# Kernel optimization log

Hardware: AMD Instinct MI355X
Metric: run time of the kernel (lower is better)

Reference implementation:

```python
import jax, jax.numpy as jnp
import numpy as np

B, L, D, H = 32, 512, 512, 8          # batch(=num_nodes), seq len, model_size, num_heads
HD = D // H                            # head size
E_DIM, N_EDGES, N_PATHS = 128, 4096, 1024  # edge_dim (hardcoded 128), edge table, #(src,dst) pairs
MAXD = H                               # max_path_distance == num_heads


def setup_inputs() -> dict:
    rng = jax.random.key(0)
    ks = jax.random.split(rng, 16)
    n = lambda k, s: jax.random.normal(k, s, jnp.float32)
    idx = jnp.arange(N_PATHS)
    inp = {
        'query': n(ks[0], (B, L, D)),
        'key':   n(ks[1], (B, L, D)),
        'value': n(ks[2], (B, L, D)),
        'mask':  jnp.ones((B, 1, 1, L), jnp.float32),
        'edge_attr': n(ks[3], (N_EDGES, E_DIM)),
        'path_src': (idx // B).astype(jnp.int32),   # all (src,dst) node pairs
        'path_dst': (idx % B).astype(jnp.int32),
        'path_edges': jax.random.randint(ks[4], (N_PATHS, MAXD), 0, N_EDGES),
        'path_lens': jax.random.randint(ks[5], (N_PATHS,), 1, MAXD + 1),
        # learned params
        'WQ': n(ks[6], (D, D)) * 0.02, 'bQ': jnp.zeros((D,), jnp.float32),
        'WK': n(ks[7], (D, D)) * 0.02, 'bK': jnp.zeros((D,), jnp.float32),
        'WV': n(ks[8], (D, D)) * 0.02, 'bV': jnp.zeros((D,), jnp.float32),
        'WO': n(ks[9], (D, D)) * 0.02, 'bO': jnp.zeros((D,), jnp.float32),
        'edge_vector': n(ks[10], (MAXD, E_DIM)) * 0.05,  # EdgeEncoding weight
        'b_vec': n(ks[11], (MAXD,)) * 0.05,              # SpatialEncoding weight
        'b_scale': jnp.float32(0.001),
        'c_scale': jnp.float32(0.001),
    }
    return inp


def reference(query, key, value, mask, edge_attr, path_src, path_dst, path_edges,
              path_lens, WQ, bQ, WK, bK, WV, bV, WO, bO, edge_vector, b_vec,
              b_scale, c_scale):
    def split_heads(x):  # [B,L,D] -> [B,H,L,HD]
        return x.reshape(B, L, H, HD).transpose(0, 2, 1, 3)

    q = split_heads(jnp.einsum('bld,de->ble', query, WQ) + bQ)
    k = split_heads(jnp.einsum('bld,de->ble', key, WK) + bK)
    v = split_heads(jnp.einsum('bld,de->ble', value, WV) + bV)

    score = jnp.einsum('bhqd,bhkd->bhqk', q, k) / jnp.sqrt(jnp.float32(HD))

    pl = jnp.minimum(path_lens, MAXD).astype(jnp.int32)  # clipped path lengths

    # SpatialEncoding: spatial[src,dst] = b_vec[min(len,maxd)-1]
    spatial = jnp.zeros((B, B), jnp.float32).at[path_src, path_dst].set(b_vec[pl - 1])
    b_mean = spatial.mean(axis=1)  # [B]

    # EdgeEncoding: cij[src,dst] = mean_k <edge_vector[k], edge_attr[path[k]]>
    pe = edge_attr[path_edges]                       # [P,MAXD,E]  batched gather
    dots = jnp.einsum('ke,pke->pk', edge_vector, pe)  # [P,MAXD]
    kmask = (jnp.arange(MAXD)[None, :] < pl[:, None]).astype(jnp.float32)
    cvals = jnp.where(pl > 0, (dots * kmask).sum(1) / jnp.maximum(pl, 1), 0.0)
    cij = jnp.zeros((B, B), jnp.float32).at[path_src, path_dst].set(cvals)
    c_mean = cij.mean(axis=1)  # [B]

    bias = (b_scale * b_mean + c_scale * c_mean)[:, None, None, None]
    score = score + bias + (1.0 - mask) * (-1e9)

    alpha = jax.nn.softmax(score, axis=-1)
    ctx = jnp.einsum('bhqk,bhkd->bhqd', alpha, v)
    ctx = ctx.transpose(0, 2, 1, 3).reshape(B, L, D)
    return jnp.einsum('bld,de->ble', ctx, WO) + bO
```

## Files before the change

### kernel.cpp

```cpp
#include <hip/hip_runtime.h>
#include <hip/hip_bf16.h>

#define B_  32
#define L_  512
#define D_  512
#define H_  8
#define HD_ 64

typedef __attribute__((ext_vector_type(8))) short bf16x8;
typedef __attribute__((ext_vector_type(4))) short bf16x4;
typedef __attribute__((ext_vector_type(4))) float f32x4;

__device__ __forceinline__ short f2bf(float f) {
  union { float f; unsigned u; } x; x.f = f;
  unsigned r = x.u + 0x7FFFu + ((x.u >> 16) & 1u);
  return (short)(r >> 16);
}

__device__ __forceinline__ void gll16(const void* g, void* l) {
  __builtin_amdgcn_global_load_lds(
      (const __attribute__((address_space(1))) unsigned int*)g,
      (__attribute__((address_space(3))) unsigned int*)l, 16, 0, 0);
}

__device__ __forceinline__ bf16x8 cvt8(f32x4 a, f32x4 b) {
  union { __hip_bfloat162 h[4]; bf16x8 v; } u;
  u.h[0] = __float22bfloat162_rn(float2{a[0], a[1]});
  u.h[1] = __float22bfloat162_rn(float2{a[2], a[3]});
  u.h[2] = __float22bfloat162_rn(float2{b[0], b[1]});
  u.h[3] = __float22bfloat162_rn(float2{b[2], b[3]});
  return u.v;
}

#define DS_FENCE() do { asm volatile("s_waitcnt lgkmcnt(0)" ::: "memory"); \
                        __builtin_amdgcn_sched_barrier(0); } while (0)

__global__ __launch_bounds__(256) void wt_kernel(
    const float* __restrict__ WQ, const float* __restrict__ WK,
    const float* __restrict__ WV, const float* __restrict__ WO,
    short* __restrict__ wt) {
  __shared__ float tile[32][33];
  int wz = blockIdx.z;
  const float* W = (wz == 0) ? WQ : (wz == 1) ? WK : (wz == 2) ? WV : WO;
  int k0 = blockIdx.y * 32, n0 = blockIdx.x * 32;
  int tr = threadIdx.x >> 5, tc = threadIdx.x & 31;
#pragma unroll
  for (int i = 0; i < 4; ++i)
    tile[tr + i * 8][tc] = W[(size_t)(k0 + tr + i * 8) * D_ + n0 + tc];
  __syncthreads();
#pragma unroll
  for (int i = 0; i < 4; ++i)
    wt[((size_t)wz * D_ + n0 + tr + i * 8) * D_ + k0 + tc] =
        f2bf(tile[tc][tr + i * 8]);
}

__global__ __launch_bounds__(256) void gemm_qkv(
    const float* __restrict__ Xq, const float* __restrict__ Xk,
    const float* __restrict__ Xv, const short* __restrict__ wt,
    const float* __restrict__ bQ, const float* __restrict__ bK,
    const float* __restrict__ bV,
    short* __restrict__ q_ws, short* __restrict__ k_ws,
    short* __restrict__ vt_ws) {
  __shared__ __align__(16) char lds[49152];
  char* Al = lds;
  char* Bl = lds + 32768;

  int mode = blockIdx.z;
  const float* A = (mode == 0) ? Xq : (mode == 1) ? Xk : Xv;
  const short* WT = wt + (size_t)mode * D_ * D_;
  const float* bias = (mode == 0) ? bQ : (mode == 1) ? bK : bV;

  int wgid = blockIdx.x + 4 * blockIdx.y;
  int rr_ = wgid >> 3;
  int m0 = ((wgid & 7) * 16 + (rr_ >> 2)) * 128;
  int n0 = (rr_ & 3) * 128;

  int tid = threadIdx.x, lane = tid & 63, w = tid >> 6;
  int wr = w >> 1, wc = w & 1, g = lane >> 4, lr = lane & 15;

  f32x4 acc[4][4] = {};

  for (int k0 = 0; k0 < D_; k0 += 64) {
    __syncthreads();
#pragma unroll
    for (int j = 0; j < 8; ++j) {
      int e = w * 8 + j;
      int row = e * 4 + (lane >> 4);
      int chunk = (lane & 15) ^ (row & 15);
      gll16(A + (size_t)(m0 + row) * D_ + k0 + chunk * 4, Al + e * 1024);
    }
#pragma unroll
    for (int j = 0; j < 4; ++j) {
      int e = w * 4 + j;
      int row = e * 8 + (lane >> 3);
      int chunk = (lane & 7) ^ (lane >> 3);
      gll16(WT + (size_t)(n0 + row) * D_ + k0 + chunk * 8, Bl + e * 1024);
    }
    __syncthreads();
#pragma unroll
    for (int kk = 0; kk < 2; ++kk) {
      bf16x8 af[4], bf_[4];
#pragma unroll
      for (int i = 0; i < 4; ++i) {
        int row = wr * 64 + i * 16 + lr;
        int o0 = ((kk * 8 + g * 2) ^ lr) << 4;
        int o1 = ((kk * 8 + g * 2 + 1) ^ lr) << 4;
        f32x4 lo = *(const f32x4*)(Al + row * 256 + o0);
        f32x4 hi = *(const f32x4*)(Al + row * 256 + o1);
        af[i] = cvt8(lo, hi);
      }
#pragma unroll
      for (int i = 0; i < 4; ++i) {
        int row = wc * 64 + i * 16 + lr;
        bf_[i] = *(const bf16x8*)(Bl + row * 128 +
                                  (((kk * 4 + g) ^ (lr & 7)) << 4));
      }
#pragma unroll
      for (int mi = 0; mi < 4; ++mi)
#pragma unroll
        for (int nj = 0; nj < 4; ++nj)
          acc[mi][nj] = __builtin_amdgcn_mfma_f32_16x16x32_bf16(
              af[mi], bf_[nj], acc[mi][nj], 0, 0, 0);
    }
  }

#pragma unroll
  for (int mi = 0; mi < 4; ++mi) {
#pragma unroll
    for (int nj = 0; nj < 4; ++nj) {
      int n = n0 + wc * 64 + nj * 16 + lr;
      float bb = bias[n];
      int h = n >> 6, hd = n & 63;
#pragma unroll
      for (int rr = 0; rr < 4; ++rr) {
        int m = m0 + wr * 64 + mi * 16 + g * 4 + rr;
        int b = m >> 9, l = m & 511;
        short v = f2bf(acc[mi][nj][rr] + bb);
        if (mode == 0)
          q_ws[(((size_t)b * H_ + h) * L_ + l) * HD_ + hd] = v;
        else if (mode == 1)
          k_ws[(((size_t)b * H_ + h) * L_ + l) * HD_ + hd] = v;
        else
          vt_ws[(((size_t)b * H_ + h) * HD_ + hd) * L_ + l] = v;
      }
    }
  }
}

__global__ __launch_bounds__(256, 4) void attn_kernel(
    const short* __restrict__ q_ws, const short* __restrict__ k_ws,
    const short* __restrict__ vt_ws, const float* __restrict__ mask,
    short* __restrict__ ctx_ws) {
  __shared__ __align__(16) char lds[40960];
  int wg = blockIdx.x;
  int bh   = (wg & 7) * 32 + (wg >> 6);
  int qblk = (wg >> 3) & 7;
  int b = bh >> 3, h = bh & 7;
  int tid = threadIdx.x, lane = tid & 63, w = tid >> 6;
  int g = lane >> 4, lr = lane & 15;
  char* Pl = lds + 32768 + w * 2048;
  int qbase = qblk * 64 + w * 16;

  const short* Qh  = q_ws  + (size_t)bh * (L_ * HD_);
  const short* Kh  = k_ws  + (size_t)bh * (L_ * HD_);
  const short* VTh = vt_ws + (size_t)bh * (HD_ * L_);
  const float* mrow = mask + (size_t)b * L_;

  bf16x8 aq0 = *(const bf16x8*)(Qh + (size_t)(qbase + lr) * HD_ + g * 8);
  bf16x8 aq1 = *(const bf16x8*)(Qh + (size_t)(qbase + lr) * HD_ + 32 + g * 8);

  int rowin = lane >> 3;
  int sch8 = ((lane & 7) ^ rowin) * 8;

#pragma unroll
  for (int j = 0; j < 2; ++j) {
    int e = w * 2 + j, row = e * 8 + rowin;
    gll16(Kh + (size_t)row * HD_ + sch8, lds + e * 1024);
    gll16(VTh + (size_t)row * L_ + sch8, lds + 16384 + e * 1024);
  }
  __syncthreads();

  f32x4 c[4] = {};
  float m[4] = {-1e30f, -1e30f, -1e30f, -1e30f};
  float sum[4] = {0.f, 0.f, 0.f, 0.f};

  for (int ch = 0; ch < 8; ++ch) {
    const char* Kb = lds + (ch & 1) * 8192;
    const char* Vb = lds + 16384 + (ch & 1) * 8192;
    if (ch < 7) {
      char* Kn = lds + ((ch + 1) & 1) * 8192;
      char* Vn = lds + 16384 + ((ch + 1) & 1) * 8192;
#pragma unroll
      for (int j = 0; j < 2; ++j) {
        int e = w * 2 + j, row = e * 8 + rowin;
        gll16(Kh + ((size_t)(ch + 1) * 64 + row) * HD_ + sch8, Kn + e * 1024);
        gll16(VTh + (size_t)row * L_ + (ch + 1) * 64 + sch8, Vn + e * 1024);
      }
    }
    float mb[4];
#pragma unroll
    for (int kt = 0; kt < 4; ++kt)
      mb[kt] = (1.0f - mrow[ch * 64 + kt * 16 + lr]) * -1e9f;

    f32x4 s[4];
#pragma unroll
    for (int kt = 0; kt < 4; ++kt) {
      int row = kt * 16 + lr;
      bf16x8 bk0 = *(const bf16x8*)(Kb + row * 128 + ((g ^ (lr & 7)) << 4));
      bf16x8 bk1 = *(const bf16x8*)(Kb + row * 128 + (((4 + g) ^ (lr & 7)) << 4));
      f32x4 a = {0.f, 0.f, 0.f, 0.f};
      a = __builtin_amdgcn_mfma_f32_16x16x32_bf16(aq0, bk0, a, 0, 0, 0);
      a = __builtin_amdgcn_mfma_f32_16x16x32_bf16(aq1, bk1, a, 0, 0, 0);
#pragma unroll
      for (int rr = 0; rr < 4; ++rr) a[rr] = a[rr] * 0.125f + mb[kt];
      s[kt] = a;
    }

    float pmax[4], scl[4];
#pragma unroll
    for (int rr = 0; rr < 4; ++rr)
      pmax[rr] = fmaxf(fmaxf(s[0][rr], s[1][rr]), fmaxf(s[2][rr], s[3][rr]));
#pragma unroll
    for (int off = 1; off < 16; off <<= 1)
#pragma unroll
      for (int rr = 0; rr < 4; ++rr)
        pmax[rr] = fmaxf(pmax[rr], __shfl_xor(pmax[rr], off, 64));
#pragma unroll
    for (int rr = 0; rr < 4; ++rr) {
      float mn = fmaxf(m[rr], pmax[rr]);
      scl[rr] = __expf(m[rr] - mn);
      m[rr] = mn;
      sum[rr] *= scl[rr];
    }
#pragma unroll
    for (int nt = 0; nt < 4; ++nt)
#pragma unroll
      for (int rr = 0; rr < 4; ++rr) c[nt][rr] *= scl[rr];

#pragma unroll
    for (int kt = 0; kt < 4; ++kt) {
      int col2 = (kt * 16 + lr) * 2;
#pragma unroll
      for (int rr = 0; rr < 4; ++rr) {
        float p = __expf(s[kt][rr] - m[rr]);
        sum[rr] += p;
        int row = g * 4 + rr;
        *(short*)(Pl + row * 128 + (col2 ^ ((row & 7) << 4))) = f2bf(p);
      }
    }
    DS_FENCE();

#pragma unroll
    for (int kk = 0; kk < 2; ++kk) {
      bf16x8 ap = *(const bf16x8*)(Pl + lr * 128 +
                                   (((kk * 4 + g) ^ (lr & 7)) << 4));
#pragma unroll
      for (int nt = 0; nt < 4; ++nt) {
        int row = nt * 16 + lr;
        bf16x8 bv = *(const bf16x8*)(Vb + row * 128 +
                                     (((kk * 4 + g) ^ (lr & 7)) << 4));
        c[nt] = __builtin_amdgcn_mfma_f32_16x16x32_bf16(ap, bv, c[nt], 0, 0, 0);
      }
    }
    DS_FENCE();
    if (ch < 7) __syncthreads();
  }

  float inv[4];
#pragma unroll
  for (int off = 1; off < 16; off <<= 1)
#pragma unroll
    for (int rr = 0; rr < 4; ++rr) sum[rr] += __shfl_xor(sum[rr], off, 64);
#pragma unroll
  for (int rr = 0; rr < 4; ++rr) inv[rr] = 1.0f / sum[rr];

#pragma unroll
  for (int nt = 0; nt < 4; ++nt) {
    int hd = nt * 16 + lr;
#pragma unroll
    for (int rr = 0; rr < 4; ++rr) {
      int qrow = qbase + g * 4 + rr;
      ctx_ws[(((size_t)b * L_ + qrow) * H_ + h) * HD_ + hd] =
          f2bf(c[nt][rr] * inv[rr]);
    }
  }
}

__global__ __launch_bounds__(256) void gemm_out(
    const short* __restrict__ ctx, const short* __restrict__ wt3,
    const float* __restrict__ bO, float* __restrict__ out) {
  __shared__ __align__(16) char lds[32768];
  char* Al = lds;
  char* Bl = lds + 16384;
  int wgid = blockIdx.x + 4 * blockIdx.y;
  int rr_ = wgid >> 3;
  int m0 = ((wgid & 7) * 16 + (rr_ >> 2)) * 128;
  int n0 = (rr_ & 3) * 128;
  int tid = threadIdx.x, lane = tid & 63, w = tid >> 6;
  int wr = w >> 1, wc = w & 1, g = lane >> 4, lr = lane & 15;
  f32x4 acc[4][4] = {};

  for (int k0 = 0; k0 < D_; k0 += 64) {
    __syncthreads();
#pragma unroll
    for (int j = 0; j < 4; ++j) {
      int e = w * 4 + j;
      int row = e * 8 + (lane >> 3);
      int chunk = (lane & 7) ^ (lane >> 3);
      gll16(ctx + (size_t)(m0 + row) * D_ + k0 + chunk * 8, Al + e * 1024);
    }
#pragma unroll
    for (int j = 0; j < 4; ++j) {
      int e = w * 4 + j;
      int row = e * 8 + (lane >> 3);
      int chunk = (lane & 7) ^ (lane >> 3);
      gll16(wt3 + (size_t)(n0 + row) * D_ + k0 + chunk * 8, Bl + e * 1024);
    }
    __syncthreads();
#pragma unroll
    for (int kk = 0; kk < 2; ++kk) {
      bf16x8 af[4], bf_[4];
#pragma unroll
      for (int i = 0; i < 4; ++i) {
        int row = wr * 64 + i * 16 + lr;
        af[i] = *(const bf16x8*)(Al + row * 128 +
                                 (((kk * 4 + g) ^ (lr & 7)) << 4));
      }
#pragma unroll
      for (int i = 0; i < 4; ++i) {
        int row = wc * 64 + i * 16 + lr;
        bf_[i] = *(const bf16x8*)(Bl + row * 128 +
                                  (((kk * 4 + g) ^ (lr & 7)) << 4));
      }
#pragma unroll
      for (int mi = 0; mi < 4; ++mi)
#pragma unroll
        for (int nj = 0; nj < 4; ++nj)
          acc[mi][nj] = __builtin_amdgcn_mfma_f32_16x16x32_bf16(
              af[mi], bf_[nj], acc[mi][nj], 0, 0, 0);
    }
  }
#pragma unroll
  for (int mi = 0; mi < 4; ++mi) {
#pragma unroll
    for (int nj = 0; nj < 4; ++nj) {
      int n = n0 + wc * 64 + nj * 16 + lr;
      float bb = bO[n];
#pragma unroll
      for (int rr = 0; rr < 4; ++rr) {
        int m = m0 + wr * 64 + mi * 16 + g * 4 + rr;
        out[(size_t)m * D_ + n] = acc[mi][nj][rr] + bb;
      }
    }
  }
}

extern "C" void kernel_launch(void* const* d_in, const int* in_sizes, int n_in,
                              void* d_out, int out_size, void* d_ws,
                              size_t ws_size, hipStream_t stream) {
  const float* query = (const float*)d_in[0];
  const float* key   = (const float*)d_in[1];
  const float* value = (const float*)d_in[2];
  const float* mask  = (const float*)d_in[3];
  const float* WQ = (const float*)d_in[9];
  const float* bQ = (const float*)d_in[10];
  const float* WK = (const float*)d_in[11];
  const float* bK = (const float*)d_in[12];
  const float* WV = (const float*)d_in[13];
  const float* bV = (const float*)d_in[14];
  const float* WO = (const float*)d_in[15];
  const float* bO = (const float*)d_in[16];

  short* ws  = (short*)d_ws;
  short* wt  = ws;
  short* q   = ws + 1048576;
  short* k   = q + 8388608;
  short* vt  = k + 8388608;
  short* ctx = vt + 8388608;
  float* out = (float*)d_out;

  wt_kernel<<<dim3(16, 16, 4), 256, 0, stream>>>(WQ, WK, WV, WO, wt);
  gemm_qkv<<<dim3(4, 128, 3), 256, 0, stream>>>(query, key, value, wt,
                                                bQ, bK, bV, q, k, vt);
  attn_kernel<<<2048, 256, 0, stream>>>(q, k, vt, mask, ctx);
  gemm_out<<<dim3(4, 128), 256, 0, stream>>>(ctx, wt + 3 * 262144, bO, out);
}
```

Measured before the change: 135.5 us.

## Load A operand directly to registers and double-buffer B tiles in LDS

Both the QKV projection and the output projection GEMMs stop staging the activation (A) tile through LDS. Each wave now loads its A fragments straight from global memory into registers, prefetching the next K-step while the current one runs on MFMA. The weight (B) tile is double-buffered in LDS, so only one barrier per K-step is needed and the next tile's load overlaps compute. This cuts LDS traffic and footprint and adds an occupancy hint of 3 blocks, at the cost of more registers held by prefetched fragments and uncoalesced-per-wave global reads of A.

```diff
diff --git a/kernel.cpp b/kernel.cpp
--- a/kernel.cpp
+++ b/kernel.cpp
@@ -54,16 +54,14 @@
         f2bf(tile[tc][tr + i * 8]);
 }
 
-__global__ __launch_bounds__(256) void gemm_qkv(
+__global__ __launch_bounds__(256, 3) void gemm_qkv(
     const float* __restrict__ Xq, const float* __restrict__ Xk,
     const float* __restrict__ Xv, const short* __restrict__ wt,
     const float* __restrict__ bQ, const float* __restrict__ bK,
     const float* __restrict__ bV,
     short* __restrict__ q_ws, short* __restrict__ k_ws,
     short* __restrict__ vt_ws) {
-  __shared__ __align__(16) char lds[49152];
-  char* Al = lds;
-  char* Bl = lds + 32768;
+  __shared__ __align__(16) char Bl[2][16384];
 
   int mode = blockIdx.z;
   const float* A = (mode == 0) ? Xq : (mode == 1) ? Xk : Xv;
@@ -77,50 +75,83 @@
 
   int tid = threadIdx.x, lane = tid & 63, w = tid >> 6;
   int wr = w >> 1, wc = w & 1, g = lane >> 4, lr = lane & 15;
+  int rowin = lane >> 3, sch8 = ((lane & 7) ^ rowin) * 8;
+
+  const float* Ab = A + (size_t)(m0 + wr * 64 + lr) * D_ + g * 8;
 
   f32x4 acc[4][4] = {};
-
-  for (int k0 = 0; k0 < D_; k0 += 64) {
+  bf16x8 acur[4][2];
+
+#pragma unroll
+  for (int j = 0; j < 4; ++j) {
+    int e = w * 4 + j, row = e * 8 + rowin;
+    gll16(WT + (size_t)(n0 + row) * D_ + sch8, &Bl[0][e * 1024]);
+  }
+#pragma unroll
+  for (int i = 0; i < 4; ++i)
+#pragma unroll
+    for (int kk = 0; kk < 2; ++kk) {
+      const float* p = Ab + (size_t)i * (16 * D_) + kk * 32;
+      acur[i][kk] = cvt8(*(const f32x4*)p, *(const f32x4*)(p + 4));
+    }
+
+#pragma unroll
+  for (int it = 0; it < 8; ++it) {
     __syncthreads();
-#pragma unroll
-    for (int j = 0; j < 8; ++j) {
-      int e = w * 8 + j;
-      int row = e * 4 + (lane >> 4);
-      int chunk = (lane & 15) ^ (row & 15);
-      gll16(A + (size_t)(m0 + row) * D_ + k0 + chunk * 4, Al + e * 1024);
-    }
-#pragma unroll
-    for (int j = 0; j < 4; ++j) {
-      int e = w * 4 + j;
-      int row = e * 8 + (lane >> 3);
-      int chunk = (lane & 7) ^ (lane >> 3);
-      gll16(WT + (size_t)(n0 + row) * D_ + k0 + chunk * 8, Bl + e * 1024);
-    }
-    __syncthreads();
-#pragma unroll
-    for (int kk = 0; kk < 2; ++kk) {
-      bf16x8 af[4], bf_[4];
+    if (it < 7) {
+#pragma unroll
+      for (int j = 0; j < 4; ++j) {
+        int e = w * 4 + j, row = e * 8 + rowin;
+        gll16(WT + (size_t)(n0 + row) * D_ + (it + 1) * 64 + sch8,
+              &Bl[(it + 1) & 1][e * 1024]);
+      }
+    }
+    f32x4 nx0[4], nx1[4], ny0[4], ny1[4];
+    if (it < 7) {
 #pragma unroll
       for (int i = 0; i < 4; ++i) {
-        int row = wr * 64 + i * 16 + lr;
-        int o0 = ((kk * 8 + g * 2) ^ lr) << 4;
-        int o1 = ((kk * 8 + g * 2 + 1) ^ lr) << 4;
-        f32x4 lo = *(const f32x4*)(Al + row * 256 + o0);
-        f32x4 hi = *(const f32x4*)(Al + row * 256 + o1);
-        af[i] = cvt8(lo, hi);
-      }
+        const float* p = Ab + (size_t)i * (16 * D_) + (it + 1) * 64;
+        nx0[i] = *(const f32x4*)p;
+        nx1[i] = *(const f32x4*)(p + 4);
+      }
+    }
+    bf16x8 bf_[4];
+#pragma unroll
+    for (int i = 0; i < 4; ++i) {
+      int row = wc * 64 + i * 16 + lr;
+      bf_[i] = *(const bf16x8*)(&Bl[it & 1][row * 128 + ((g ^ (lr & 7)) << 4)]);
+    }
+#pragma unroll
+    for (int mi = 0; mi < 4; ++mi)
+#pragma unroll
+      for (int nj = 0; nj < 4; ++nj)
+        acc[mi][nj] = __builtin_amdgcn_mfma_f32_16x16x32_bf16(
+            acur[mi][0], bf_[nj], acc[mi][nj], 0, 0, 0);
+    if (it < 7) {
+#pragma unroll
+      for (int i = 0; i < 4; ++i) acur[i][0] = cvt8(nx0[i], nx1[i]);
 #pragma unroll
       for (int i = 0; i < 4; ++i) {
-        int row = wc * 64 + i * 16 + lr;
-        bf_[i] = *(const bf16x8*)(Bl + row * 128 +
-                                  (((kk * 4 + g) ^ (lr & 7)) << 4));
-      }
-#pragma unroll
-      for (int mi = 0; mi < 4; ++mi)
-#pragma unroll
-        for (int nj = 0; nj < 4; ++nj)
-          acc[mi][nj] = __builtin_amdgcn_mfma_f32_16x16x32_bf16(
-              af[mi], bf_[nj], acc[mi][nj], 0, 0, 0);
+        const float* p = Ab + (size_t)i * (16 * D_) + (it + 1) * 64 + 32;
+        ny0[i] = *(const f32x4*)p;
+        ny1[i] = *(const f32x4*)(p + 4);
+      }
+    }
+#pragma unroll
+    for (int i = 0; i < 4; ++i) {
+      int row = wc * 64 + i * 16 + lr;
+      bf_[i] = *(const bf16x8*)(&Bl[it & 1][row * 128 +
+                                           (((4 + g) ^ (lr & 7)) << 4)]);
+    }
+#pragma unroll
+    for (int mi = 0; mi < 4; ++mi)
+#pragma unroll
+      for (int nj = 0; nj < 4; ++nj)
+        acc[mi][nj] = __builtin_amdgcn_mfma_f32_16x16x32_bf16(
+            acur[mi][1], bf_[nj], acc[mi][nj], 0, 0, 0);
+    if (it < 7) {
+#pragma unroll
+      for (int i = 0; i < 4; ++i) acur[i][1] = cvt8(ny0[i], ny1[i]);
     }
   }
 
@@ -286,58 +317,72 @@
   }
 }
 
-__global__ __launch_bounds__(256) void gemm_out(
+__global__ __launch_bounds__(256, 3) void gemm_out(
     const short* __restrict__ ctx, const short* __restrict__ wt3,
     const float* __restrict__ bO, float* __restrict__ out) {
-  __shared__ __align__(16) char lds[32768];
-  char* Al = lds;
-  char* Bl = lds + 16384;
+  __shared__ __align__(16) char Bl[2][16384];
   int wgid = blockIdx.x + 4 * blockIdx.y;
   int rr_ = wgid >> 3;
   int m0 = ((wgid & 7) * 16 + (rr_ >> 2)) * 128;
   int n0 = (rr_ & 3) * 128;
   int tid = threadIdx.x, lane = tid & 63, w = tid >> 6;
   int wr = w >> 1, wc = w & 1, g = lane >> 4, lr = lane & 15;
+  int rowin = lane >> 3, sch8 = ((lane & 7) ^ rowin) * 8;
+
+  const short* Ab = ctx + (size_t)(m0 + wr * 64 + lr) * D_ + g * 8;
+
   f32x4 acc[4][4] = {};
-
-  for (int k0 = 0; k0 < D_; k0 += 64) {
+  bf16x8 acur[4][2], anxt[4][2];
+
+#pragma unroll
+  for (int j = 0; j < 4; ++j) {
+    int e = w * 4 + j, row = e * 8 + rowin;
+    gll16(wt3 + (size_t)(n0 + row) * D_ + sch8, &Bl[0][e * 1024]);
+  }
+#pragma unroll
+  for (int i = 0; i < 4; ++i)
+#pragma unroll
+    for (int kk = 0; kk < 2; ++kk)
+      acur[i][kk] = *(const bf16x8*)(Ab + (size_t)i * (16 * D_) + kk * 32);
+
+#pragma unroll
+  for (int it = 0; it < 8; ++it) {
     __syncthreads();
-#pragma unroll
-    for (int j = 0; j < 4; ++j) {
-      int e = w * 4 + j;
-      int row = e * 8 + (lane >> 3);
-      int chunk = (lane & 7) ^ (lane >> 3);
-      gll16(ctx + (size_t)(m0 + row) * D_ + k0 + chunk * 8, Al + e * 1024);
-    }
-#pragma unroll
-    for (int j = 0; j < 4; ++j) {
-      int e = w * 4 + j;
-      int row = e * 8 + (lane >> 3);
-      int chunk = (lane & 7) ^ (lane >> 3);
-      gll16(wt3 + (size_t)(n0 + row) * D_ + k0 + chunk * 8, Bl + e * 1024);
-    }
-    __syncthreads();
+    if (it < 7) {
+#pragma unroll
+      for (int j = 0; j < 4; ++j) {
+        int e = w * 4 + j, row = e * 8 + rowin;
+        gll16(wt3 + (size_t)(n0 + row) * D_ + (it + 1) * 64 + sch8,
+              &Bl[(it + 1) & 1][e * 1024]);
+      }
+#pragma unroll
+      for (int i = 0; i < 4; ++i)
+#pragma unroll
+        for (int kk = 0; kk < 2; ++kk)
+          anxt[i][kk] = *(const bf16x8*)(Ab + (size_t)i * (16 * D_) +
+                                         (it + 1) * 64 + kk * 32);
+    }
 #pragma unroll
     for (int kk = 0; kk < 2; ++kk) {
-      bf16x8 af[4], bf_[4];
-#pragma unroll
-      for (int i = 0; i < 4; ++i) {
-        int row = wr * 64 + i * 16 + lr;
-        af[i] = *(const bf16x8*)(Al + row * 128 +
-                                 (((kk * 4 + g) ^ (lr & 7)) << 4));
-      }
+      bf16x8 bf_[4];
 #pragma unroll
       for (int i = 0; i < 4; ++i) {
         int row = wc * 64 + i * 16 + lr;
-        bf_[i] = *(const bf16x8*)(Bl + row * 128 +
-                                  (((kk * 4 + g) ^ (lr & 7)) << 4));
+        bf_[i] = *(const bf16x8*)(&Bl[it & 1][row * 128 +
+                                             (((kk * 4 + g) ^ (lr & 7)) << 4)]);
       }
 #pragma unroll
       for (int mi = 0; mi < 4; ++mi)
 #pragma unroll
         for (int nj = 0; nj < 4; ++nj)
           acc[mi][nj] = __builtin_amdgcn_mfma_f32_16x16x32_bf16(
-              af[mi], bf_[nj], acc[mi][nj], 0, 0, 0);
+              acur[mi][kk], bf_[nj], acc[mi][nj], 0, 0, 0);
+    }
+    if (it < 7) {
+#pragma unroll
+      for (int i = 0; i < 4; ++i)
+#pragma unroll
+        for (int kk = 0; kk < 2; ++kk) acur[i][kk] = anxt[i][kk];
     }
   }
 #pragma unroll
```

Measured after the change: 190.3 us. 1.41x slower.

## Double-buffer LDS staging in QKV and output GEMMs with smaller K tiles

Applied to the files above, without the earlier changes.

Both projection GEMMs now use a two-stage LDS ping-pong with a K step of 32 instead of 64. The next tile's global-to-LDS loads are issued before the MFMAs on the current tile, which removes one barrier per iteration and overlaps memory with compute. The swizzle patterns are rewritten for the narrower rows, and launch bounds now request 3 waves per SIMD. The loop runs more iterations with less work each, and the occupancy hint may add register pressure.

```diff
diff --git a/kernel.cpp b/kernel.cpp
--- a/kernel.cpp
+++ b/kernel.cpp
@@ -54,7 +54,7 @@
         f2bf(tile[tc][tr + i * 8]);
 }
 
-__global__ __launch_bounds__(256) void gemm_qkv(
+__global__ __launch_bounds__(256, 3) void gemm_qkv(
     const float* __restrict__ Xq, const float* __restrict__ Xk,
     const float* __restrict__ Xv, const short* __restrict__ wt,
     const float* __restrict__ bQ, const float* __restrict__ bK,
@@ -62,8 +62,6 @@
     short* __restrict__ q_ws, short* __restrict__ k_ws,
     short* __restrict__ vt_ws) {
   __shared__ __align__(16) char lds[49152];
-  char* Al = lds;
-  char* Bl = lds + 32768;
 
   int mode = blockIdx.z;
   const float* A = (mode == 0) ? Xq : (mode == 1) ? Xk : Xv;
@@ -78,50 +76,53 @@
   int tid = threadIdx.x, lane = tid & 63, w = tid >> 6;
   int wr = w >> 1, wc = w & 1, g = lane >> 4, lr = lane & 15;
 
+  int qa = lane >> 3, ca = (lane & 7) ^ qa;
+  int qb = lane >> 2, cb = (lane & 3) ^ ((lane >> 3) & 3);
+
+  auto stage = [&](int ks, int bs) {
+    char* Ab = lds + bs * 16384;
+    char* Bb = lds + 32768 + bs * 8192;
+#pragma unroll
+    for (int j = 0; j < 4; ++j) {
+      int e = w * 4 + j, row = e * 8 + qa;
+      gll16(A + (size_t)(m0 + row) * D_ + ks * 32 + ca * 4, Ab + e * 1024);
+    }
+#pragma unroll
+    for (int j = 0; j < 2; ++j) {
+      int e = w * 2 + j, row = e * 16 + qb;
+      gll16(WT + (size_t)(n0 + row) * D_ + ks * 32 + cb * 8, Bb + e * 1024);
+    }
+  };
+
+  stage(0, 0);
+  __syncthreads();
+
   f32x4 acc[4][4] = {};
-
-  for (int k0 = 0; k0 < D_; k0 += 64) {
+#pragma unroll
+  for (int ks = 0; ks < 16; ++ks) {
+    if (ks < 15) stage(ks + 1, (ks + 1) & 1);
+    const char* Ab = lds + (ks & 1) * 16384;
+    const char* Bb = lds + 32768 + (ks & 1) * 8192;
+    bf16x8 af[4], bf_[4];
+#pragma unroll
+    for (int i = 0; i < 4; ++i) {
+      int row = wr * 64 + i * 16 + lr;
+      f32x4 lo = *(const f32x4*)(Ab + row * 128 + (((2 * g) ^ (lr & 7)) << 4));
+      f32x4 hi = *(const f32x4*)(Ab + row * 128 + (((2 * g + 1) ^ (lr & 7)) << 4));
+      af[i] = cvt8(lo, hi);
+    }
+#pragma unroll
+    for (int i = 0; i < 4; ++i) {
+      int row = wc * 64 + i * 16 + lr;
+      bf_[i] = *(const bf16x8*)(Bb + row * 64 + ((g ^ ((lr >> 1) & 3)) << 4));
+    }
+#pragma unroll
+    for (int mi = 0; mi < 4; ++mi)
+#pragma unroll
+      for (int nj = 0; nj < 4; ++nj)
+        acc[mi][nj] = __builtin_amdgcn_mfma_f32_16x16x32_bf16(
+            af[mi], bf_[nj], acc[mi][nj], 0, 0, 0);
     __syncthreads();
-#pragma unroll
-    for (int j = 0; j < 8; ++j) {
-      int e = w * 8 + j;
-      int row = e * 4 + (lane >> 4);
-      int chunk = (lane & 15) ^ (row & 15);
-      gll16(A + (size_t)(m0 + row) * D_ + k0 + chunk * 4, Al + e * 1024);
-    }
-#pragma unroll
-    for (int j = 0; j < 4; ++j) {
-      int e = w * 4 + j;
-      int row = e * 8 + (lane >> 3);
-      int chunk = (lane & 7) ^ (lane >> 3);
-      gll16(WT + (size_t)(n0 + row) * D_ + k0 + chunk * 8, Bl + e * 1024);
-    }
-    __syncthreads();
-#pragma unroll
-    for (int kk = 0; kk < 2; ++kk) {
-      bf16x8 af[4], bf_[4];
-#pragma unroll
-      for (int i = 0; i < 4; ++i) {
-        int row = wr * 64 + i * 16 + lr;
-        int o0 = ((kk * 8 + g * 2) ^ lr) << 4;
-        int o1 = ((kk * 8 + g * 2 + 1) ^ lr) << 4;
-        f32x4 lo = *(const f32x4*)(Al + row * 256 + o0);
-        f32x4 hi = *(const f32x4*)(Al + row * 256 + o1);
-        af[i] = cvt8(lo, hi);
-      }
-#pragma unroll
-      for (int i = 0; i < 4; ++i) {
-        int row = wc * 64 + i * 16 + lr;
-        bf_[i] = *(const bf16x8*)(Bl + row * 128 +
-                                  (((kk * 4 + g) ^ (lr & 7)) << 4));
-      }
-#pragma unroll
-      for (int mi = 0; mi < 4; ++mi)
-#pragma unroll
-        for (int nj = 0; nj < 4; ++nj)
-          acc[mi][nj] = __builtin_amdgcn_mfma_f32_16x16x32_bf16(
-              af[mi], bf_[nj], acc[mi][nj], 0, 0, 0);
-    }
   }
 
 #pragma unroll
@@ -286,59 +287,56 @@
   }
 }
 
-__global__ __launch_bounds__(256) void gemm_out(
+__global__ __launch_bounds__(256, 3) void gemm_out(
     const short* __restrict__ ctx, const short* __restrict__ wt3,
     const float* __restrict__ bO, float* __restrict__ out) {
   __shared__ __align__(16) char lds[32768];
-  char* Al = lds;
-  char* Bl = lds + 16384;
   int wgid = blockIdx.x + 4 * blockIdx.y;
   int rr_ = wgid >> 3;
   int m0 = ((wgid & 7) * 16 + (rr_ >> 2)) * 128;
   int n0 = (rr_ & 3) * 128;
   int tid = threadIdx.x, lane = tid & 63, w = tid >> 6;
   int wr = w >> 1, wc = w & 1, g = lane >> 4, lr = lane & 15;
+  int qb = lane >> 2, cb = (lane & 3) ^ ((lane >> 3) & 3);
+
+  auto stage = [&](int ks, int bs) {
+    char* Ab = lds + bs * 8192;
+    char* Bb = lds + 16384 + bs * 8192;
+#pragma unroll
+    for (int j = 0; j < 2; ++j) {
+      int e = w * 2 + j, row = e * 16 + qb;
+      gll16(ctx + (size_t)(m0 + row) * D_ + ks * 32 + cb * 8, Ab + e * 1024);
+      gll16(wt3 + (size_t)(n0 + row) * D_ + ks * 32 + cb * 8, Bb + e * 1024);
+    }
+  };
+
+  stage(0, 0);
+  __syncthreads();
+
   f32x4 acc[4][4] = {};
-
-  for (int k0 = 0; k0 < D_; k0 += 64) {
+#pragma unroll
+  for (int ks = 0; ks < 16; ++ks) {
+    if (ks < 15) stage(ks + 1, (ks + 1) & 1);
+    const char* Ab = lds + (ks & 1) * 8192;
+    const char* Bb = lds + 16384 + (ks & 1) * 8192;
+    bf16x8 af[4], bf_[4];
+#pragma unroll
+    for (int i = 0; i < 4; ++i) {
+      int row = wr * 64 + i * 16 + lr;
+      af[i] = *(const bf16x8*)(Ab + row * 64 + ((g ^ ((lr >> 1) & 3)) << 4));
+    }
+#pragma unroll
+    for (int i = 0; i < 4; ++i) {
+      int row = wc * 64 + i * 16 + lr;
+      bf_[i] = *(const bf16x8*)(Bb + row * 64 + ((g ^ ((lr >> 1) & 3)) << 4));
+    }
+#pragma unroll
+    for (int mi = 0; mi < 4; ++mi)
+#pragma unroll
+      for (int nj = 0; nj < 4; ++nj)
+        acc[mi][nj] = __builtin_amdgcn_mfma_f32_16x16x32_bf16(
+            af[mi], bf_[nj], acc[mi][nj], 0, 0, 0);
     __syncthreads();
-#pragma unroll
-    for (int j = 0; j < 4; ++j) {
-      int e = w * 4 + j;
-      int row = e * 8 + (lane >> 3);
-      int chunk = (lane & 7) ^ (lane >> 3);
-      gll16(ctx + (size_t)(m0 + row) * D_ + k0 + chunk * 8, Al + e * 1024);
-    }
-#pragma unroll
-    for (int j = 0; j < 4; ++j) {
-      int e = w * 4 + j;
-      int row = e * 8 + (lane >> 3);
-      int chunk = (lane & 7) ^ (lane >> 3);
-      gll16(wt3 + (size_t)(n0 + row) * D_ + k0 + chunk * 8, Bl + e * 1024);
-    }
-    __syncthreads();
-#pragma unroll
-    for (int kk = 0; kk < 2; ++kk) {
-      bf16x8 af[4], bf_[4];
-#pragma unroll
-      for (int i = 0; i < 4; ++i) {
-        int row = wr * 64 + i * 16 + lr;
-        af[i] = *(const bf16x8*)(Al + row * 128 +
-                                 (((kk * 4 + g) ^ (lr & 7)) << 4));
-      }
-#pragma unroll
-      for (int i = 0; i < 4; ++i) {
-        int row = wc * 64 + i * 16 + lr;
-        bf_[i] = *(const bf16x8*)(Bl + row * 128 +
-                                  (((kk * 4 + g) ^ (lr & 7)) << 4));
-      }
-#pragma unroll
-      for (int mi = 0; mi < 4; ++mi)
-#pragma unroll
-        for (int nj = 0; nj < 4; ++nj)
-          acc[mi][nj] = __builtin_amdgcn_mfma_f32_16x16x32_bf16(
-              af[mi], bf_[nj], acc[mi][nj], 0, 0, 0);
-    }
   }
 #pragma unroll
   for (int mi = 0; mi < 4; ++mi) {
```

Result: no change. 133.0 us (-1.8%).
